# Kernel optimization log

Hardware: AMD Instinct MI355X
Metric: run time of the kernel (lower is better)

The kernel has to match this reference:

```python
import jax, jax.numpy as jnp
import numpy as np

IN_NC = 7


def setup_inputs() -> dict:
    key = jax.random.key(0)
    ks = jax.random.split(key, 32)
    B, H, W = 4, 192, 192
    Cf, O, L = 64, 64, 32  # in_fea, out_fea, len=max(64//16,32)
    d = {}
    d['fea'] = jax.random.normal(ks[0], (B, Cf, H, W), jnp.float32)
    d['inputs'] = jax.random.normal(ks[1], (B, IN_NC, H, W), jnp.float32)
    j = 2
    for i in range(3):
        k = 2 * i + 1
        oc = IN_NC * 3 * k * k
        d['dw_w%d' % i] = jax.random.normal(ks[j], (Cf, 1, k, k), jnp.float32) * 0.05; j += 1
        d['dw_b%d' % i] = jnp.zeros((Cf,), jnp.float32)
        d['pw_w%d' % i] = jax.random.normal(ks[j], (oc, Cf), jnp.float32) * 0.05; j += 1
        d['pw_b%d' % i] = jnp.zeros((oc,), jnp.float32)
        d['dcn_w%d' % i] = jax.random.normal(ks[j], (O, IN_NC, k, k), jnp.float32) * 0.05; j += 1
        d['dcn_b%d' % i] = jnp.zeros((O,), jnp.float32)
    d['attn_w'] = jax.random.normal(ks[j], (O, 3 * O), jnp.float32) * 0.05; j += 1
    d['attn_b'] = jnp.zeros((O,), jnp.float32)
    d['fc_w'] = jax.random.normal(ks[j], (L, O), jnp.float32) * 0.05; j += 1
    d['fc_b'] = jnp.zeros((L,), jnp.float32)
    for i in range(3):
        d['fcs_w%d' % i] = jax.random.normal(ks[j], (O, L), jnp.float32) * 0.05; j += 1
        d['fcs_b%d' % i] = jnp.zeros((O,), jnp.float32)
    d['conv_w'] = jax.random.normal(ks[j], (O, 3 * O), jnp.float32) * 0.05; j += 1
    d['conv_b'] = jnp.zeros((O,), jnp.float32)
    return d


def _dw_conv(x, w, b):
    # depthwise conv, stride 1, SAME padding (pad = k//2 for odd k)
    y = jax.lax.conv_general_dilated(x, w, window_strides=(1, 1), padding='SAME',
                                     dimension_numbers=('NCHW', 'OIHW', 'NCHW'),
                                     feature_group_count=x.shape[1])
    return y + b[None, :, None, None]


def _pw_conv(x, w, b):
    return jnp.einsum('bchw,oc->bohw', x, w) + b[None, :, None, None]


def _mdcn(x, offset, mask, w, b, k):
    # Modulated deformable conv, deformable_groups == C (one channel per group),
    # stride 1, padding k//2. offset: [B, C*2*K, H, W] as (c, k, (dy,dx)); mask: [B, C*K, H, W].
    B, C, H, W = x.shape
    K = k * k
    pad = k // 2
    off = offset.reshape(B, C, K, 2, H, W)
    m = mask.reshape(B, C, K, H, W)
    ky = (jnp.arange(K) // k).astype(jnp.float32)
    kx = (jnp.arange(K) % k).astype(jnp.float32)
    py = off[:, :, :, 0] + (ky[:, None, None] + jnp.arange(H, dtype=jnp.float32)[None, :, None] - pad)
    px = off[:, :, :, 1] + (kx[:, None, None] + jnp.arange(W, dtype=jnp.float32)[None, None, :] - pad)
    y0 = jnp.floor(py)
    x0 = jnp.floor(px)
    wy = py - y0
    wx = px - x0
    bi = jnp.arange(B)[:, None, None, None, None]
    ci = jnp.arange(C)[None, :, None, None, None]

    def gather(yi, xi):
        valid = (yi >= 0) & (yi < H) & (xi >= 0) & (xi < W)
        yc = jnp.clip(yi, 0, H - 1).astype(jnp.int32)
        xc = jnp.clip(xi, 0, W - 1).astype(jnp.int32)
        return jnp.where(valid, x[bi, ci, yc, xc], 0.0)

    v00 = gather(y0, x0)
    v01 = gather(y0, x0 + 1)
    v10 = gather(y0 + 1, x0)
    v11 = gather(y0 + 1, x0 + 1)
    samp = (v00 * (1 - wy) * (1 - wx) + v01 * (1 - wy) * wx
            + v10 * wy * (1 - wx) + v11 * wy * wx) * m  # [B,C,K,H,W]
    O = w.shape[0]
    return jnp.einsum('bckhw,ock->bohw', samp, w.reshape(O, C, K)) + b[None, :, None, None]


def reference(fea, inputs,
              dw_w0, dw_b0, pw_w0, pw_b0, dcn_w0, dcn_b0,
              dw_w1, dw_b1, pw_w1, pw_b1, dcn_w1, dcn_b1,
              dw_w2, dw_b2, pw_w2, pw_b2, dcn_w2, dcn_b2,
              attn_w, attn_b, fc_w, fc_b,
              fcs_w0, fcs_b0, fcs_w1, fcs_b1, fcs_w2, fcs_b2,
              conv_w, conv_b):
    dw_w = [dw_w0, dw_w1, dw_w2]; dw_b = [dw_b0, dw_b1, dw_b2]
    pw_w = [pw_w0, pw_w1, pw_w2]; pw_b = [pw_b0, pw_b1, pw_b2]
    dcn_w = [dcn_w0, dcn_w1, dcn_w2]; dcn_b = [dcn_b0, dcn_b1, dcn_b2]
    fcs_w = [fcs_w0, fcs_w1, fcs_w2]; fcs_b = [fcs_b0, fcs_b1, fcs_b2]
    outs = []
    for i in range(3):
        k = 2 * i + 1
        ds = k * k
        om = _pw_conv(_dw_conv(fea, dw_w[i], dw_b[i]), pw_w[i], pw_b[i])
        offset = om[:, :IN_NC * 2 * ds]
        mask = jax.nn.sigmoid(om[:, IN_NC * 2 * ds:])
        outs.append(jax.nn.relu(_mdcn(inputs, offset, mask, dcn_w[i], dcn_b[i], k)))
    out = jnp.stack(outs, axis=1)  # [B, 3, O, H, W]
    B, T, C, H, W = out.shape
    att = jax.nn.relu(_pw_conv(out.reshape(B, T * C, H, W), attn_w, attn_b))
    att = jnp.mean(att, axis=(2, 3), keepdims=True)  # GAP -> [B, O, 1, 1]
    att = jax.nn.relu(_pw_conv(att, fc_w, fc_b))      # [B, L, 1, 1]
    atts = jnp.stack([_pw_conv(att, fcs_w[i], fcs_b[i]) for i in range(3)], axis=1)  # [B,3,O,1,1]
    out = out * atts
    out = jax.nn.relu(_pw_conv(out.reshape(B, T * C, H, W), conv_w, conv_b))
    return out
```

## Files before the change

kernel.cpp:

```cpp
#include <hip/hip_runtime.h>
#include <math.h>

#define HH 192
#define WW 192
#define HWP (192*192)
#define BB 4
#define CF 64
#define NC 7
#define OO 64
#define NTOT (BB*HWP)
#define PBLK2 (HWP/128)

typedef float f32x4 __attribute__((ext_vector_type(4)));

template<int k>
__global__ __launch_bounds__(256)
void dwv_kernel(const float* __restrict__ fea, const float* __restrict__ w,
                const float* __restrict__ bias, float* __restrict__ out) {
    constexpr int pad = k / 2;
    int idx = blockIdx.x * 256 + threadIdx.x;
    int xq = idx % 48;
    int x0 = xq * 4;
    int hpos = (idx / 48) % HH;
    int plane = idx / (48 * HH);
    int c = plane % CF;
    const float* f = fea + (size_t)plane * HWP;

    float wk[k * k];
#pragma unroll
    for (int i = 0; i < k * k; ++i) wk[i] = w[c * k * k + i];

    float acc0 = 0.f, acc1 = 0.f, acc2 = 0.f, acc3 = 0.f;
#pragma unroll
    for (int dy = 0; dy < k; ++dy) {
        int y = hpos + dy - pad;
        if (y < 0 || y >= HH) continue;
        const float* row = f + y * WW;
        float4 q0 = (x0 >= 4) ? *(const float4*)(row + x0 - 4) : make_float4(0.f, 0.f, 0.f, 0.f);
        float4 q1 = *(const float4*)(row + x0);
        float4 q2 = (x0 + 4 < WW) ? *(const float4*)(row + x0 + 4) : make_float4(0.f, 0.f, 0.f, 0.f);
        float wnd[8] = {q0.z, q0.w, q1.x, q1.y, q1.z, q1.w, q2.x, q2.y};
#pragma unroll
        for (int dx = 0; dx < k; ++dx) {
            float wt = wk[dy * k + dx];
            acc0 += wnd[0 + dx + 2 - pad] * wt;
            acc1 += wnd[1 + dx + 2 - pad] * wt;
            acc2 += wnd[2 + dx + 2 - pad] * wt;
            acc3 += wnd[3 + dx + 2 - pad] * wt;
        }
    }
    float b = bias[c];
    float4 o = make_float4(acc0 + b, acc1 + b, acc2 + b, acc3 + b);
    *(float4*)(out + (size_t)plane * HWP + hpos * WW + x0) = o;
}

__global__ void transpose_kernel(const float* __restrict__ in, float* __restrict__ out,
                                 int rows, int cols) {
    int idx = blockIdx.x * 256 + threadIdx.x;
    if (idx >= rows * cols) return;
    int r = idx / cols, c = idx % cols;
    out[c * rows + r] = in[idx];
}

__global__ void k1_fold_kernel(const float* __restrict__ pw_w, const float* __restrict__ pw_b,
                               const float* __restrict__ dw_w0, const float* __restrict__ dw_b0,
                               float* __restrict__ pw_wf, float* __restrict__ pw_bf) {
    int i = blockIdx.x * 256 + threadIdx.x;
    if (i < 21 * 64) pw_wf[i] = pw_w[i] * dw_w0[i & 63];
    if (i < 21) {
        float s = pw_b[i];
        for (int c = 0; c < 64; ++c) s += pw_w[i * 64 + c] * dw_b0[c];
        pw_bf[i] = s;
    }
}

template<int k>
__global__ __launch_bounds__(256)
void branch_fused_kernel(const float* __restrict__ pw_w, const float* __restrict__ pw_b,
                         const float* __restrict__ dw, const float* __restrict__ inputs,
                         const float* __restrict__ dcn_wt, const float* __restrict__ dcn_b,
                         float* __restrict__ outbuf, int t_slot) {
    constexpr int K = k * k;
    constexpr int TT = NC * K;
    constexpr int pad = k / 2;
    __shared__ float As[64][68];
    __shared__ float Bs[64][68];
    __shared__ float Cs[64][68];
    int nb0 = blockIdx.x * 64;
    int b = nb0 / HWP, p0 = nb0 % HWP;
    int tid = threadIdx.x;
    int tm = (tid & 15) * 4;
    int tn = (tid >> 4) * 4;
    int h0 = 0, w0 = 0;

    {
        const float* bp = dw + (size_t)b * CF * HWP + p0;
        for (int i4 = tid; i4 < 64 * 16; i4 += 256) {
            int kk = i4 >> 4, f4 = (i4 & 15) * 4;
            float4 v = *(const float4*)(bp + (size_t)kk * HWP + f4);
            *(float4*)&Bs[kk][f4] = v;
        }
    }

    f32x4 acc0 = 0.f, acc1 = 0.f, acc2 = 0.f, acc3 = 0.f;
    const float* inb = inputs + (size_t)b * NC * HWP;

    for (int tap0 = 0; tap0 < TT; tap0 += 21) {
        int ntap = (TT - tap0 < 21) ? (TT - tap0) : 21;
        int M = 3 * ntap;
        __syncthreads();
        {
            int m = tid & 63;
            int kq = tid >> 6;
            if (m < M) {
                int i = m / 3, q = m - 3 * i;
                int r = tap0 + i;
                int srow = (q == 2) ? (2 * TT + r) : (2 * r + q);
                const float* ap = pw_w + (size_t)srow * CF;
#pragma unroll
                for (int i2 = 0; i2 < 4; ++i2) {
                    int k0 = (kq * 4 + i2) * 4;
                    float4 v = *(const float4*)(ap + k0);
                    As[k0 + 0][m] = v.x; As[k0 + 1][m] = v.y;
                    As[k0 + 2][m] = v.z; As[k0 + 3][m] = v.w;
                }
            }
        }
        __syncthreads();
        f32x4 c0 = 0.f, c1 = 0.f, c2 = 0.f, c3 = 0.f;
#pragma unroll 8
        for (int kk = 0; kk < 64; ++kk) {
            f32x4 a = *(const f32x4*)&As[kk][tm];
            f32x4 bv = *(const f32x4*)&Bs[kk][tn];
#pragma unroll
            for (int j = 0; j < 4; ++j) {
                c0[j] += a[0] * bv[j]; c1[j] += a[1] * bv[j];
                c2[j] += a[2] * bv[j]; c3[j] += a[3] * bv[j];
            }
        }
        {
            f32x4 cs[4] = {c0, c1, c2, c3};
#pragma unroll
            for (int r2 = 0; r2 < 4; ++r2) {
                int m = tm + r2;
                if (m < M) {
                    int i = m / 3, q = m - 3 * i;
                    int r = tap0 + i;
                    float bi = pw_b[(q == 2) ? (2 * TT + r) : (2 * r + q)];
                    f32x4 v = cs[r2];
#pragma unroll
                    for (int j = 0; j < 4; ++j) v[j] += bi;
                    *(f32x4*)&Cs[m][tn] = v;
                }
            }
        }
        __syncthreads();
        for (int i4 = tid; i4 < ntap * 16; i4 += 256) {
            int row = i4 >> 4, c4 = (i4 & 15) * 4;
            float4 v = *(const float4*)(dcn_wt + (size_t)(tap0 + row) * OO + c4);
            *(float4*)&As[row][c4] = v;
        }
        {
            int px = tid & 63;
            int p = p0 + px;
            int h = p / WW, wq = p % WW;
            for (int i = tid >> 6; i < ntap; i += 4) {
                int r = tap0 + i;
                float oy = Cs[3 * i][px];
                float ox = Cs[3 * i + 1][px];
                float mr = Cs[3 * i + 2][px];
                int c = r / K;
                int kk2 = r - c * K;
                int ky = kk2 / k, kx = kk2 - ky * k;
                const float* inc_ = inb + (size_t)c * HWP;
                float m = 1.f / (1.f + __expf(-mr));
                float py = oy + (float)(ky + h - pad);
                float px_ = ox + (float)(kx + wq - pad);
                float y0 = floorf(py), x0 = floorf(px_);
                float wyf = py - y0, wxf = px_ - x0;
                int iy0 = (int)y0, ix0 = (int)x0;
                bool y0v = (iy0 >= 0) && (iy0 < HH);
                bool y1v = (iy0 + 1 >= 0) && (iy0 + 1 < HH);
                bool x0v = (ix0 >= 0) && (ix0 < WW);
                bool x1v = (ix0 + 1 >= 0) && (ix0 + 1 < WW);
                int yc0 = min(max(iy0, 0), HH - 1), yc1 = min(max(iy0 + 1, 0), HH - 1);
                int xc0 = min(max(ix0, 0), WW - 1), xc1 = min(max(ix0 + 1, 0), WW - 1);
                float v00 = 0.f, v01 = 0.f, v10 = 0.f, v11 = 0.f;
                if (y0v) {
                    if (x0v) v00 = inc_[yc0 * WW + xc0];
                    if (x1v) v01 = inc_[yc0 * WW + xc1];
                }
                if (y1v) {
                    if (x0v) v10 = inc_[yc1 * WW + xc0];
                    if (x1v) v11 = inc_[yc1 * WW + xc1];
                }
                float s = (v00 * (1.f - wyf) * (1.f - wxf) + v01 * (1.f - wyf) * wxf +
                           v10 * wyf * (1.f - wxf) + v11 * wyf * wxf) * m;
                Cs[3 * i][px] = s;
            }
        }
        __syncthreads();
        for (int kk = 0; kk < ntap; ++kk) {
            f32x4 a = *(const f32x4*)&As[kk][tm];
            f32x4 s = *(const f32x4*)&Cs[3 * kk][tn];
#pragma unroll
            for (int j = 0; j < 4; ++j) {
                acc0[j] += a[0] * s[j]; acc1[j] += a[1] * s[j];
                acc2[j] += a[2] * s[j]; acc3[j] += a[3] * s[j];
            }
        }
    }
    __syncthreads();
    {
        f32x4 accs[4] = {acc0, acc1, acc2, acc3};
#pragma unroll
        for (int r2 = 0; r2 < 4; ++r2) {
            int ch = tm + r2;
            float bi = dcn_b[ch];
            f32x4 v = accs[r2];
#pragma unroll
            for (int j = 0; j < 4; ++j) {
                v[j] += bi;
                v[j] = v[j] > 0.f ? v[j] : 0.f;
            }
            *(f32x4*)&Cs[ch][tn] = v;
        }
    }
    __syncthreads();
    {
        float* op = outbuf + (size_t)((b * 3 + t_slot) * OO) * HWP + p0;
        for (int i4 = tid; i4 < 64 * 16; i4 += 256) {
            int row = i4 >> 4, f4 = (i4 & 15) * 4;
            *(float4*)(op + (size_t)row * HWP + f4) = *(const float4*)&Cs[row][f4];
        }
    }
}

__global__ __launch_bounds__(256)
void attn_gemm_kernel(const float* __restrict__ outbuf, const float* __restrict__ attn_wt,
                      const float* __restrict__ attn_b, float* __restrict__ partial) {
    __shared__ float As[32][68];
    __shared__ float Bs[32][132];
    __shared__ float red[16][68];
    int nb0 = blockIdx.x * 128;
    int b = nb0 / HWP, p0 = nb0 % HWP;
    int tid = threadIdx.x;
    int tm = (tid & 15) * 4;
    int tn = (tid >> 4) * 8;

    f32x4 aA0 = 0.f, aA1 = 0.f, aB0 = 0.f, aB1 = 0.f;
    f32x4 aC0 = 0.f, aC1 = 0.f, aD0 = 0.f, aD1 = 0.f;
    for (int kc = 0; kc < 6; ++kc) {
        for (int i4 = tid; i4 < 32 * 16; i4 += 256) {
            int row = i4 >> 4, c4 = (i4 & 15) * 4;
            float4 v = *(const float4*)(attn_wt + (size_t)(kc * 32 + row) * OO + c4);
            As[row][c4] = v.x; As[row][c4 + 1] = v.y; As[row][c4 + 2] = v.z; As[row][c4 + 3] = v.w;
        }
        const float* bp = outbuf + ((size_t)(b * 192 + kc * 32)) * HWP + p0;
        for (int i4 = tid; i4 < 32 * 32; i4 += 256) {
            int row = i4 >> 5, f4 = (i4 & 31) * 4;
            float4 v = *(const float4*)(bp + (size_t)row * HWP + f4);
            *(float4*)&Bs[row][f4] = v;
        }
        __syncthreads();
#pragma unroll 4
        for (int kk = 0; kk < 32; ++kk) {
            f32x4 a  = *(const f32x4*)&As[kk][tm];
            f32x4 b0 = *(const f32x4*)&Bs[kk][tn];
            f32x4 b1 = *(const f32x4*)&Bs[kk][tn + 4];
#pragma unroll
            for (int j = 0; j < 4; ++j) {
                aA0[j] += a[0] * b0[j];  aA1[j] += a[0] * b1[j];
                aB0[j] += a[1] * b0[j];  aB1[j] += a[1] * b1[j];
                aC0[j] += a[2] * b0[j];  aC1[j] += a[2] * b1[j];
                aD0[j] += a[3] * b0[j];  aD1[j] += a[3] * b1[j];
            }
        }
        __syncthreads();
    }
    float bsum[4];
    {
        f32x4 accs[8] = {aA0, aA1, aB0, aB1, aC0, aC1, aD0, aD1};
#pragma unroll
        for (int row = 0; row < 4; ++row) {
            float bi = attn_b[tm + row];
            float s = 0.f;
#pragma unroll
            for (int j = 0; j < 4; ++j) {
                float v0 = accs[row * 2][j] + bi;
                float v1 = accs[row * 2 + 1][j] + bi;
                s += (v0 > 0.f ? v0 : 0.f) + (v1 > 0.f ? v1 : 0.f);
            }
            bsum[row] = s;
        }
    }
    int pg = tid >> 4;
#pragma unroll
    for (int row = 0; row < 4; ++row) red[pg][tm + row] = bsum[row];
    __syncthreads();
    if (tid < 64) {
        float s = 0.f;
#pragma unroll
        for (int g = 0; g < 16; ++g) s += red[g][tid];
        int lb = p0 / 128;
        partial[((size_t)(b * PBLK2 + lb)) * OO + tid] = s;
    }
}

__global__ void attn_finish_kernel(const float* __restrict__ partial,
                                   const float* __restrict__ fc_w, const float* __restrict__ fc_b,
                                   const float* __restrict__ fcs_w0, const float* __restrict__ fcs_b0,
                                   const float* __restrict__ fcs_w1, const float* __restrict__ fcs_b1,
                                   const float* __restrict__ fcs_w2, const float* __restrict__ fcs_b2,
                                   float* __restrict__ atts) {
    int b = blockIdx.x;
    __shared__ float attm[OO];
    __shared__ float fcv[32];
    int tid = threadIdx.x;
    if (tid < OO) {
        float s = 0.f;
        for (int blk = 0; blk < PBLK2; ++blk)
            s += partial[((size_t)(b * PBLK2 + blk)) * OO + tid];
        attm[tid] = s / (float)HWP;
    }
    __syncthreads();
    if (tid < 32) {
        float s = fc_b[tid];
        for (int o = 0; o < OO; ++o) s += fc_w[tid * OO + o] * attm[o];
        fcv[tid] = s > 0.f ? s : 0.f;
    }
    __syncthreads();
    if (tid < OO) {
        {
            float s = fcs_b0[tid];
            for (int j = 0; j < 32; ++j) s += fcs_w0[tid * 32 + j] * fcv[j];
            atts[b * 192 + 0 * OO + tid] = s;
        }
        {
            float s = fcs_b1[tid];
            for (int j = 0; j < 32; ++j) s += fcs_w1[tid * 32 + j] * fcv[j];
            atts[b * 192 + 1 * OO + tid] = s;
        }
        {
            float s = fcs_b2[tid];
            for (int j = 0; j < 32; ++j) s += fcs_w2[tid * 32 + j] * fcv[j];
            atts[b * 192 + 2 * OO + tid] = s;
        }
    }
}

__global__ __launch_bounds__(256)
void final_gemm_kernel(const float* __restrict__ outbuf, const float* __restrict__ atts,
                       const float* __restrict__ conv_wt, const float* __restrict__ conv_b,
                       float* __restrict__ out) {
    __shared__ float As[32][68];
    __shared__ float Bs[32][132];
    int nb0 = blockIdx.x * 128;
    int b = nb0 / HWP, p0 = nb0 % HWP;
    int tid = threadIdx.x;
    int tm = (tid & 15) * 4;
    int tn = (tid >> 4) * 8;
    const float* at = atts + b * 192;

    f32x4 aA0 = 0.f, aA1 = 0.f, aB0 = 0.f, aB1 = 0.f;
    f32x4 aC0 = 0.f, aC1 = 0.f, aD0 = 0.f, aD1 = 0.f;
    for (int kc = 0; kc < 6; ++kc) {
        for (int i4 = tid; i4 < 32 * 16; i4 += 256) {
            int row = i4 >> 4, c4 = (i4 & 15) * 4;
            float4 v = *(const float4*)(conv_wt + (size_t)(kc * 32 + row) * OO + c4);
            As[row][c4] = v.x; As[row][c4 + 1] = v.y; As[row][c4 + 2] = v.z; As[row][c4 + 3] = v.w;
        }
        const float* bp = outbuf + ((size_t)(b * 192 + kc * 32)) * HWP + p0;
        for (int i4 = tid; i4 < 32 * 32; i4 += 256) {
            int row = i4 >> 5, f4 = (i4 & 31) * 4;
            float sc = at[kc * 32 + row];
            float4 v = *(const float4*)(bp + (size_t)row * HWP + f4);
            Bs[row][f4] = v.x * sc; Bs[row][f4 + 1] = v.y * sc;
            Bs[row][f4 + 2] = v.z * sc; Bs[row][f4 + 3] = v.w * sc;
        }
        __syncthreads();
#pragma unroll 4
        for (int kk = 0; kk < 32; ++kk) {
            f32x4 a  = *(const f32x4*)&As[kk][tm];
            f32x4 b0 = *(const f32x4*)&Bs[kk][tn];
            f32x4 b1 = *(const f32x4*)&Bs[kk][tn + 4];
#pragma unroll
            for (int j = 0; j < 4; ++j) {
                aA0[j] += a[0] * b0[j];  aA1[j] += a[0] * b1[j];
                aB0[j] += a[1] * b0[j];  aB1[j] += a[1] * b1[j];
                aC0[j] += a[2] * b0[j];  aC1[j] += a[2] * b1[j];
                aD0[j] += a[3] * b0[j];  aD1[j] += a[3] * b1[j];
            }
        }
        __syncthreads();
    }
    f32x4 accs[8] = {aA0, aA1, aB0, aB1, aC0, aC1, aD0, aD1};
#pragma unroll
    for (int row = 0; row < 4; ++row) {
        int ch = tm + row;
        float bi = conv_b[ch];
        float* ptr = out + ((size_t)(b * OO + ch)) * HWP + p0 + tn;
        f32x4 lo = accs[row * 2], hi = accs[row * 2 + 1];
#pragma unroll
        for (int j = 0; j < 4; ++j) {
            lo[j] += bi; hi[j] += bi;
            lo[j] = lo[j] > 0.f ? lo[j] : 0.f;
            hi[j] = hi[j] > 0.f ? hi[j] : 0.f;
        }
        *(f32x4*)ptr = lo;
        *(f32x4*)(ptr + 4) = hi;
    }
}

extern "C" void kernel_launch(void* const* d_in, const int* in_sizes, int n_in,
                              void* d_out, int out_size, void* d_ws, size_t ws_size,
                              hipStream_t stream) {
    const float* fea    = (const float*)d_in[0];
    const float* inputs = (const float*)d_in[1];
    const float* dw_w[3]  = {(const float*)d_in[2],  (const float*)d_in[8],  (const float*)d_in[14]};
    const float* dw_b[3]  = {(const float*)d_in[3],  (const float*)d_in[9],  (const float*)d_in[15]};
    const float* pw_w[3]  = {(const float*)d_in[4],  (const float*)d_in[10], (const float*)d_in[16]};
    const float* pw_b[3]  = {(const float*)d_in[5],  (const float*)d_in[11], (const float*)d_in[17]};
    const float* dcn_w[3] = {(const float*)d_in[6],  (const float*)d_in[12], (const float*)d_in[18]};
    const float* dcn_b[3] = {(const float*)d_in[7],  (const float*)d_in[13], (const float*)d_in[19]};
    const float* attn_w = (const float*)d_in[20];
    const float* attn_b = (const float*)d_in[21];
    const float* fc_w   = (const float*)d_in[22];
    const float* fc_b   = (const float*)d_in[23];
    const float* fcs_w[3] = {(const float*)d_in[24], (const float*)d_in[26], (const float*)d_in[28]};
    const float* fcs_b[3] = {(const float*)d_in[25], (const float*)d_in[27], (const float*)d_in[29]};
    const float* conv_w = (const float*)d_in[30];
    const float* conv_b = (const float*)d_in[31];
    float* out = (float*)d_out;

    const size_t F_OUTBUF = (size_t)BB * 3 * OO * HWP;
    float* W = (float*)d_ws;
    float* outbuf = W;            W += F_OUTBUF;
    float* partial = W;           W += 73728;
    float* atts = W;              W += 768;
    float* dcn_wt0 = W;           W += 512;
    float* dcn_wt1 = W;           W += 4096;
    float* dcn_wt2 = W;           W += 11264;
    float* attn_wt = W;           W += 12288;
    float* conv_wt = W;           W += 12288;
    float* pw_wf = W;             W += 1344;
    float* pw_bf = W;             W += 32;
    float* dwscr = out;

    transpose_kernel<<<(192 * 64 + 255) / 256, 256, 0, stream>>>(attn_w, attn_wt, 64, 192);
    transpose_kernel<<<(192 * 64 + 255) / 256, 256, 0, stream>>>(conv_w, conv_wt, 64, 192);
    transpose_kernel<<<(7 * 64 + 255) / 256, 256, 0, stream>>>(dcn_w[0], dcn_wt0, 64, 7);
    transpose_kernel<<<(63 * 64 + 255) / 256, 256, 0, stream>>>(dcn_w[1], dcn_wt1, 64, 63);
    transpose_kernel<<<(175 * 64 + 255) / 256, 256, 0, stream>>>(dcn_w[2], dcn_wt2, 64, 175);
    k1_fold_kernel<<<(21 * 64 + 255) / 256, 256, 0, stream>>>(pw_w[0], pw_b[0],
                                                              dw_w[0], dw_b[0], pw_wf, pw_bf);

    const int dwv_grid = (BB * CF * HH * 48) / 256;
    const int fuse_grid = NTOT / 64;

    dwv_kernel<5><<<dwv_grid, 256, 0, stream>>>(fea, dw_w[2], dw_b[2], dwscr);
    branch_fused_kernel<5><<<fuse_grid, 256, 0, stream>>>(
        pw_w[2], pw_b[2], dwscr, inputs, dcn_wt2, dcn_b[2], outbuf, 2);
    dwv_kernel<3><<<dwv_grid, 256, 0, stream>>>(fea, dw_w[1], dw_b[1], dwscr);
    branch_fused_kernel<3><<<fuse_grid, 256, 0, stream>>>(
        pw_w[1], pw_b[1], dwscr, inputs, dcn_wt1, dcn_b[1], outbuf, 1);
    branch_fused_kernel<1><<<fuse_grid, 256, 0, stream>>>(
        pw_wf, pw_bf, fea, inputs, dcn_wt0, dcn_b[0], outbuf, 0);

    attn_gemm_kernel<<<NTOT / 128, 256, 0, stream>>>(outbuf, attn_wt, attn_b, partial);
    attn_finish_kernel<<<BB, 64, 0, stream>>>(partial, fc_w, fc_b,
                                              fcs_w[0], fcs_b[0], fcs_w[1], fcs_b[1],
                                              fcs_w[2], fcs_b[2], atts);
    final_gemm_kernel<<<NTOT / 128, 256, 0, stream>>>(outbuf, atts, conv_wt, conv_b, out);
}
```

Measured before the change: 613.5 us.

## Widen fused branch tile to 128 pixels and alias Cs onto Bs

Measured after the change: 653.7 us. +6.5%, slower.

```diff
diff --git a/kernel.cpp b/kernel.cpp
--- a/kernel.cpp
+++ b/kernel.cpp
@@ -84,31 +84,28 @@
     constexpr int TT = NC * K;
     constexpr int pad = k / 2;
     __shared__ float As[64][68];
-    __shared__ float Bs[64][68];
-    __shared__ float Cs[64][68];
-    int nb0 = blockIdx.x * 64;
+    __shared__ float Bs[64][132];
+    int nb0 = blockIdx.x * 128;
     int b = nb0 / HWP, p0 = nb0 % HWP;
     int tid = threadIdx.x;
     int tm = (tid & 15) * 4;
-    int tn = (tid >> 4) * 4;
-    int h0 = 0, w0 = 0;
-
-    {
-        const float* bp = dw + (size_t)b * CF * HWP + p0;
-        for (int i4 = tid; i4 < 64 * 16; i4 += 256) {
-            int kk = i4 >> 4, f4 = (i4 & 15) * 4;
-            float4 v = *(const float4*)(bp + (size_t)kk * HWP + f4);
-            *(float4*)&Bs[kk][f4] = v;
-        }
-    }
-
-    f32x4 acc0 = 0.f, acc1 = 0.f, acc2 = 0.f, acc3 = 0.f;
+    int tn = (tid >> 4) * 8;
+
     const float* inb = inputs + (size_t)b * NC * HWP;
+    f32x4 pa0 = 0.f, pa1 = 0.f, pa2 = 0.f, pa3 = 0.f;
+    f32x4 pb0 = 0.f, pb1 = 0.f, pb2 = 0.f, pb3 = 0.f;
 
     for (int tap0 = 0; tap0 < TT; tap0 += 21) {
         int ntap = (TT - tap0 < 21) ? (TT - tap0) : 21;
         int M = 3 * ntap;
         __syncthreads();
+        {
+            const float* bp = dw + (size_t)b * CF * HWP + p0;
+            for (int i4 = tid; i4 < 64 * 32; i4 += 256) {
+                int kk = i4 >> 5, f4 = (i4 & 31) * 4;
+                *(float4*)&Bs[kk][f4] = *(const float4*)(bp + (size_t)kk * HWP + f4);
+            }
+        }
         {
             int m = tid & 63;
             int kq = tid >> 6;
@@ -127,19 +124,25 @@
             }
         }
         __syncthreads();
-        f32x4 c0 = 0.f, c1 = 0.f, c2 = 0.f, c3 = 0.f;
+        f32x4 c0l = 0.f, c0h = 0.f, c1l = 0.f, c1h = 0.f;
+        f32x4 c2l = 0.f, c2h = 0.f, c3l = 0.f, c3h = 0.f;
 #pragma unroll 8
         for (int kk = 0; kk < 64; ++kk) {
-            f32x4 a = *(const f32x4*)&As[kk][tm];
-            f32x4 bv = *(const f32x4*)&Bs[kk][tn];
-#pragma unroll
-            for (int j = 0; j < 4; ++j) {
-                c0[j] += a[0] * bv[j]; c1[j] += a[1] * bv[j];
-                c2[j] += a[2] * bv[j]; c3[j] += a[3] * bv[j];
-            }
-        }
-        {
-            f32x4 cs[4] = {c0, c1, c2, c3};
+            f32x4 a  = *(const f32x4*)&As[kk][tm];
+            f32x4 b0 = *(const f32x4*)&Bs[kk][tn];
+            f32x4 b1 = *(const f32x4*)&Bs[kk][tn + 4];
+#pragma unroll
+            for (int j = 0; j < 4; ++j) {
+                c0l[j] += a[0] * b0[j];  c0h[j] += a[0] * b1[j];
+                c1l[j] += a[1] * b0[j];  c1h[j] += a[1] * b1[j];
+                c2l[j] += a[2] * b0[j];  c2h[j] += a[2] * b1[j];
+                c3l[j] += a[3] * b0[j];  c3h[j] += a[3] * b1[j];
+            }
+        }
+        __syncthreads();
+        {
+            f32x4 cl[4] = {c0l, c1l, c2l, c3l};
+            f32x4 ch[4] = {c0h, c1h, c2h, c3h};
 #pragma unroll
             for (int r2 = 0; r2 < 4; ++r2) {
                 int m = tm + r2;
@@ -147,28 +150,28 @@
                     int i = m / 3, q = m - 3 * i;
                     int r = tap0 + i;
                     float bi = pw_b[(q == 2) ? (2 * TT + r) : (2 * r + q)];
-                    f32x4 v = cs[r2];
-#pragma unroll
-                    for (int j = 0; j < 4; ++j) v[j] += bi;
-                    *(f32x4*)&Cs[m][tn] = v;
+                    f32x4 vl = cl[r2], vh = ch[r2];
+#pragma unroll
+                    for (int j = 0; j < 4; ++j) { vl[j] += bi; vh[j] += bi; }
+                    *(f32x4*)&Bs[m][tn] = vl;
+                    *(f32x4*)&Bs[m][tn + 4] = vh;
                 }
             }
         }
-        __syncthreads();
         for (int i4 = tid; i4 < ntap * 16; i4 += 256) {
             int row = i4 >> 4, c4 = (i4 & 15) * 4;
-            float4 v = *(const float4*)(dcn_wt + (size_t)(tap0 + row) * OO + c4);
-            *(float4*)&As[row][c4] = v;
-        }
-        {
-            int px = tid & 63;
+            *(float4*)&As[row][c4] = *(const float4*)(dcn_wt + (size_t)(tap0 + row) * OO + c4);
+        }
+        __syncthreads();
+        {
+            int px = tid & 127;
             int p = p0 + px;
             int h = p / WW, wq = p % WW;
-            for (int i = tid >> 6; i < ntap; i += 4) {
+            for (int i = tid >> 7; i < ntap; i += 2) {
                 int r = tap0 + i;
-                float oy = Cs[3 * i][px];
-                float ox = Cs[3 * i + 1][px];
-                float mr = Cs[3 * i + 2][px];
+                float oy = Bs[3 * i][px];
+                float ox = Bs[3 * i + 1][px];
+                float mr = Bs[3 * i + 2][px];
                 int c = r / K;
                 int kk2 = r - c * K;
                 int ky = kk2 / k, kx = kk2 - ky * k;
@@ -196,42 +199,48 @@
                 }
                 float s = (v00 * (1.f - wyf) * (1.f - wxf) + v01 * (1.f - wyf) * wxf +
                            v10 * wyf * (1.f - wxf) + v11 * wyf * wxf) * m;
-                Cs[3 * i][px] = s;
+                Bs[3 * i][px] = s;
             }
         }
         __syncthreads();
         for (int kk = 0; kk < ntap; ++kk) {
-            f32x4 a = *(const f32x4*)&As[kk][tm];
-            f32x4 s = *(const f32x4*)&Cs[3 * kk][tn];
-#pragma unroll
-            for (int j = 0; j < 4; ++j) {
-                acc0[j] += a[0] * s[j]; acc1[j] += a[1] * s[j];
-                acc2[j] += a[2] * s[j]; acc3[j] += a[3] * s[j];
+            f32x4 a  = *(const f32x4*)&As[kk][tm];
+            f32x4 s0 = *(const f32x4*)&Bs[3 * kk][tn];
+            f32x4 s1 = *(const f32x4*)&Bs[3 * kk][tn + 4];
+#pragma unroll
+            for (int j = 0; j < 4; ++j) {
+                pa0[j] += a[0] * s0[j];  pb0[j] += a[0] * s1[j];
+                pa1[j] += a[1] * s0[j];  pb1[j] += a[1] * s1[j];
+                pa2[j] += a[2] * s0[j];  pb2[j] += a[2] * s1[j];
+                pa3[j] += a[3] * s0[j];  pb3[j] += a[3] * s1[j];
             }
         }
     }
     __syncthreads();
     {
-        f32x4 accs[4] = {acc0, acc1, acc2, acc3};
+        f32x4 al[4] = {pa0, pa1, pa2, pa3};
+        f32x4 ah[4] = {pb0, pb1, pb2, pb3};
 #pragma unroll
         for (int r2 = 0; r2 < 4; ++r2) {
             int ch = tm + r2;
             float bi = dcn_b[ch];
-            f32x4 v = accs[r2];
-#pragma unroll
-            for (int j = 0; j < 4; ++j) {
-                v[j] += bi;
-                v[j] = v[j] > 0.f ? v[j] : 0.f;
-            }
-            *(f32x4*)&Cs[ch][tn] = v;
+            f32x4 vl = al[r2], vh = ah[r2];
+#pragma unroll
+            for (int j = 0; j < 4; ++j) {
+                vl[j] += bi; vh[j] += bi;
+                vl[j] = vl[j] > 0.f ? vl[j] : 0.f;
+                vh[j] = vh[j] > 0.f ? vh[j] : 0.f;
+            }
+            *(f32x4*)&Bs[ch][tn] = vl;
+            *(f32x4*)&Bs[ch][tn + 4] = vh;
         }
     }
     __syncthreads();
     {
         float* op = outbuf + (size_t)((b * 3 + t_slot) * OO) * HWP + p0;
-        for (int i4 = tid; i4 < 64 * 16; i4 += 256) {
-            int row = i4 >> 4, f4 = (i4 & 15) * 4;
-            *(float4*)(op + (size_t)row * HWP + f4) = *(const float4*)&Cs[row][f4];
+        for (int i4 = tid; i4 < 64 * 32; i4 += 256) {
+            int row = i4 >> 5, f4 = (i4 & 31) * 4;
+            *(float4*)(op + (size_t)row * HWP + f4) = *(const float4*)&Bs[row][f4];
         }
     }
 }
@@ -456,7 +465,7 @@
                                                               dw_w[0], dw_b[0], pw_wf, pw_bf);
 
     const int dwv_grid = (BB * CF * HH * 48) / 256;
-    const int fuse_grid = NTOT / 64;
+    const int fuse_grid = NTOT / 128;
 
     dwv_kernel<5><<<dwv_grid, 256, 0, stream>>>(fea, dw_w[2], dw_b[2], dwscr);
     branch_fused_kernel<5><<<fuse_grid, 256, 0, stream>>>(
```

## Widen fused branch kernel to 128 pixels with swizzled shared buffer reuse

Applied to the files above, without the earlier changes.

Result: slower. 685.6 us (+11.8%).

```diff
diff --git a/kernel.cpp b/kernel.cpp
--- a/kernel.cpp
+++ b/kernel.cpp
@@ -10,6 +10,8 @@
 #define OO 64
 #define NTOT (BB*HWP)
 #define PBLK2 (HWP/128)
+
+#define SW(r, c) ((c) ^ ((((r) >> 2) & 7) << 2))
 
 typedef float f32x4 __attribute__((ext_vector_type(4)));
 
@@ -75,7 +77,7 @@
 }
 
 template<int k>
-__global__ __launch_bounds__(256)
+__global__ __launch_bounds__(512)
 void branch_fused_kernel(const float* __restrict__ pw_w, const float* __restrict__ pw_b,
                          const float* __restrict__ dw, const float* __restrict__ inputs,
                          const float* __restrict__ dcn_wt, const float* __restrict__ dcn_b,
@@ -84,31 +86,27 @@
     constexpr int TT = NC * K;
     constexpr int pad = k / 2;
     __shared__ float As[64][68];
-    __shared__ float Bs[64][68];
-    __shared__ float Cs[64][68];
-    int nb0 = blockIdx.x * 64;
+    __shared__ float Bs[64][132];
+    int nb0 = blockIdx.x * 128;
     int b = nb0 / HWP, p0 = nb0 % HWP;
     int tid = threadIdx.x;
     int tm = (tid & 15) * 4;
-    int tn = (tid >> 4) * 4;
-    int h0 = 0, w0 = 0;
-
-    {
-        const float* bp = dw + (size_t)b * CF * HWP + p0;
-        for (int i4 = tid; i4 < 64 * 16; i4 += 256) {
-            int kk = i4 >> 4, f4 = (i4 & 15) * 4;
-            float4 v = *(const float4*)(bp + (size_t)kk * HWP + f4);
-            *(float4*)&Bs[kk][f4] = v;
-        }
-    }
-
-    f32x4 acc0 = 0.f, acc1 = 0.f, acc2 = 0.f, acc3 = 0.f;
+    int tn = ((tid >> 4) & 31) * 4;
+
     const float* inb = inputs + (size_t)b * NC * HWP;
+    f32x4 pa0 = 0.f, pa1 = 0.f, pa2 = 0.f, pa3 = 0.f;
 
     for (int tap0 = 0; tap0 < TT; tap0 += 21) {
         int ntap = (TT - tap0 < 21) ? (TT - tap0) : 21;
         int M = 3 * ntap;
         __syncthreads();
+        {
+            const float* bp = dw + (size_t)b * CF * HWP + p0;
+            for (int i4 = tid; i4 < 64 * 32; i4 += 512) {
+                int kk = i4 >> 5, f4 = (i4 & 31) * 4;
+                *(float4*)&Bs[kk][SW(kk, f4)] = *(const float4*)(bp + (size_t)kk * HWP + f4);
+            }
+        }
         {
             int m = tid & 63;
             int kq = tid >> 6;
@@ -118,8 +116,8 @@
                 int srow = (q == 2) ? (2 * TT + r) : (2 * r + q);
                 const float* ap = pw_w + (size_t)srow * CF;
 #pragma unroll
-                for (int i2 = 0; i2 < 4; ++i2) {
-                    int k0 = (kq * 4 + i2) * 4;
+                for (int i2 = 0; i2 < 2; ++i2) {
+                    int k0 = kq * 8 + i2 * 4;
                     float4 v = *(const float4*)(ap + k0);
                     As[k0 + 0][m] = v.x; As[k0 + 1][m] = v.y;
                     As[k0 + 2][m] = v.z; As[k0 + 3][m] = v.w;
@@ -130,14 +128,15 @@
         f32x4 c0 = 0.f, c1 = 0.f, c2 = 0.f, c3 = 0.f;
 #pragma unroll 8
         for (int kk = 0; kk < 64; ++kk) {
-            f32x4 a = *(const f32x4*)&As[kk][tm];
-            f32x4 bv = *(const f32x4*)&Bs[kk][tn];
+            f32x4 a  = *(const f32x4*)&As[kk][tm];
+            f32x4 bv = *(const f32x4*)&Bs[kk][SW(kk, tn)];
 #pragma unroll
             for (int j = 0; j < 4; ++j) {
                 c0[j] += a[0] * bv[j]; c1[j] += a[1] * bv[j];
                 c2[j] += a[2] * bv[j]; c3[j] += a[3] * bv[j];
             }
         }
+        __syncthreads();
         {
             f32x4 cs[4] = {c0, c1, c2, c3};
 #pragma unroll
@@ -150,25 +149,24 @@
                     f32x4 v = cs[r2];
 #pragma unroll
                     for (int j = 0; j < 4; ++j) v[j] += bi;
-                    *(f32x4*)&Cs[m][tn] = v;
+                    *(f32x4*)&Bs[m][SW(m, tn)] = v;
                 }
             }
         }
-        __syncthreads();
-        for (int i4 = tid; i4 < ntap * 16; i4 += 256) {
+        for (int i4 = tid; i4 < ntap * 16; i4 += 512) {
             int row = i4 >> 4, c4 = (i4 & 15) * 4;
-            float4 v = *(const float4*)(dcn_wt + (size_t)(tap0 + row) * OO + c4);
-            *(float4*)&As[row][c4] = v;
-        }
-        {
-            int px = tid & 63;
+            *(float4*)&As[row][c4] = *(const float4*)(dcn_wt + (size_t)(tap0 + row) * OO + c4);
+        }
+        __syncthreads();
+        {
+            int px = tid & 127;
             int p = p0 + px;
             int h = p / WW, wq = p % WW;
-            for (int i = tid >> 6; i < ntap; i += 4) {
+            for (int i = tid >> 7; i < ntap; i += 4) {
                 int r = tap0 + i;
-                float oy = Cs[3 * i][px];
-                float ox = Cs[3 * i + 1][px];
-                float mr = Cs[3 * i + 2][px];
+                float oy = Bs[3 * i][SW(3 * i, px)];
+                float ox = Bs[3 * i + 1][SW(3 * i + 1, px)];
+                float mr = Bs[3 * i + 2][SW(3 * i + 2, px)];
                 int c = r / K;
                 int kk2 = r - c * K;
                 int ky = kk2 / k, kx = kk2 - ky * k;
@@ -196,23 +194,23 @@
                 }
                 float s = (v00 * (1.f - wyf) * (1.f - wxf) + v01 * (1.f - wyf) * wxf +
                            v10 * wyf * (1.f - wxf) + v11 * wyf * wxf) * m;
-                Cs[3 * i][px] = s;
+                Bs[3 * i][SW(3 * i, px)] = s;
             }
         }
         __syncthreads();
         for (int kk = 0; kk < ntap; ++kk) {
             f32x4 a = *(const f32x4*)&As[kk][tm];
-            f32x4 s = *(const f32x4*)&Cs[3 * kk][tn];
-#pragma unroll
-            for (int j = 0; j < 4; ++j) {
-                acc0[j] += a[0] * s[j]; acc1[j] += a[1] * s[j];
-                acc2[j] += a[2] * s[j]; acc3[j] += a[3] * s[j];
+            f32x4 s = *(const f32x4*)&Bs[3 * kk][SW(3 * kk, tn)];
+#pragma unroll
+            for (int j = 0; j < 4; ++j) {
+                pa0[j] += a[0] * s[j]; pa1[j] += a[1] * s[j];
+                pa2[j] += a[2] * s[j]; pa3[j] += a[3] * s[j];
             }
         }
     }
     __syncthreads();
     {
-        f32x4 accs[4] = {acc0, acc1, acc2, acc3};
+        f32x4 accs[4] = {pa0, pa1, pa2, pa3};
 #pragma unroll
         for (int r2 = 0; r2 < 4; ++r2) {
             int ch = tm + r2;
@@ -223,15 +221,15 @@
                 v[j] += bi;
                 v[j] = v[j] > 0.f ? v[j] : 0.f;
             }
-            *(f32x4*)&Cs[ch][tn] = v;
+            *(f32x4*)&Bs[ch][SW(ch, tn)] = v;
         }
     }
     __syncthreads();
     {
         float* op = outbuf + (size_t)((b * 3 + t_slot) * OO) * HWP + p0;
-        for (int i4 = tid; i4 < 64 * 16; i4 += 256) {
-            int row = i4 >> 4, f4 = (i4 & 15) * 4;
-            *(float4*)(op + (size_t)row * HWP + f4) = *(const float4*)&Cs[row][f4];
+        for (int i4 = tid; i4 < 64 * 32; i4 += 512) {
+            int row = i4 >> 5, f4 = (i4 & 31) * 4;
+            *(float4*)(op + (size_t)row * HWP + f4) = *(const float4*)&Bs[row][SW(row, f4)];
         }
     }
 }
@@ -456,15 +454,15 @@
                                                               dw_w[0], dw_b[0], pw_wf, pw_bf);
 
     const int dwv_grid = (BB * CF * HH * 48) / 256;
-    const int fuse_grid = NTOT / 64;
+    const int fuse_grid = NTOT / 128;
 
     dwv_kernel<5><<<dwv_grid, 256, 0, stream>>>(fea, dw_w[2], dw_b[2], dwscr);
-    branch_fused_kernel<5><<<fuse_grid, 256, 0, stream>>>(
+    branch_fused_kernel<5><<<fuse_grid, 512, 0, stream>>>(
         pw_w[2], pw_b[2], dwscr, inputs, dcn_wt2, dcn_b[2], outbuf, 2);
     dwv_kernel<3><<<dwv_grid, 256, 0, stream>>>(fea, dw_w[1], dw_b[1], dwscr);
-    branch_fused_kernel<3><<<fuse_grid, 256, 0, stream>>>(
+    branch_fused_kernel<3><<<fuse_grid, 512, 0, stream>>>(
         pw_w[1], pw_b[1], dwscr, inputs, dcn_wt1, dcn_b[1], outbuf, 1);
-    branch_fused_kernel<1><<<fuse_grid, 256, 0, stream>>>(
+    branch_fused_kernel<1><<<fuse_grid, 512, 0, stream>>>(
         pw_wf, pw_bf, fea, inputs, dcn_wt0, dcn_b[0], outbuf, 0);
 
     attn_gemm_kernel<<<NTOT / 128, 256, 0, stream>>>(outbuf, attn_wt, attn_b, partial);
```
